# Performance work log

Hardware: AMD Instinct MI355X
Metric: run time of the kernel (lower is better)

Reference implementation:

```python
import jax, jax.numpy as jnp
import numpy as np

D_MODEL = 512
NHEAD = 4
HEAD_DIM = D_MODEL // NHEAD


def setup_inputs() -> dict:
    key = jax.random.key(0)
    ks = jax.random.split(key, 12)
    B, S = 2, 4096
    s = 1.0 / np.sqrt(D_MODEL)
    inp = {
        "query": jax.random.normal(ks[0], (B, S, D_MODEL), jnp.float32),
        "key": jax.random.normal(ks[1], (B, S, D_MODEL), jnp.float32),
        "value": jax.random.normal(ks[2], (B, S, D_MODEL), jnp.float32),
        "Wq": jax.random.uniform(ks[3], (D_MODEL, D_MODEL), jnp.float32, -s, s),
        "bq": jax.random.uniform(ks[4], (D_MODEL,), jnp.float32, -s, s),
        "Wk": jax.random.uniform(ks[5], (D_MODEL, D_MODEL), jnp.float32, -s, s),
        "bk": jax.random.uniform(ks[6], (D_MODEL,), jnp.float32, -s, s),
        "Wv": jax.random.uniform(ks[7], (D_MODEL, D_MODEL), jnp.float32, -s, s),
        "bv": jax.random.uniform(ks[8], (D_MODEL,), jnp.float32, -s, s),
        "Wo": jax.random.uniform(ks[9], (D_MODEL, D_MODEL), jnp.float32, -s, s),
        "bo": jax.random.uniform(ks[10], (D_MODEL,), jnp.float32, -s, s),
    }
    return inp


def reference(query, key, value, Wq, bq, Wk, bk, Wv, bv, Wo, bo):
    B, Sq, _ = query.shape
    Sk = key.shape[1]
    # projections (torch Linear: x @ W.T + b); split heads -> [B, H, S, hd]
    def proj(x, W, b, S):
        return (x @ W.T + b).reshape(B, S, NHEAD, HEAD_DIM).transpose(0, 2, 1, 3)
    Q = proj(query, Wq, bq, Sq)
    K = proj(key, Wk, bk, Sk)
    V = proj(value, Wv, bv, Sk)
    scale = 1.0 / np.sqrt(HEAD_DIM).astype(np.float32)
    scores = jnp.einsum("bhqd,bhkd->bhqk", Q, K) * scale  # [B,H,Sq,Sk]
    weights = jax.nn.softmax(scores, axis=-1)
    out = jnp.einsum("bhqk,bhkd->bhqd", weights, V)  # [B,H,Sq,hd]
    out = out.transpose(0, 2, 1, 3).reshape(B, Sq, D_MODEL)
    return out @ Wo.T + bo
```

## Files before the change

### kernel.cpp

```cpp
#include <hip/hip_runtime.h>


#define D_MODEL 512
#define NHEAD 4
#define HD 128
#define S_ 4096

typedef __attribute__((ext_vector_type(8))) short bf16x8;
typedef __attribute__((ext_vector_type(4))) short bf16x4;
typedef __attribute__((ext_vector_type(4))) float f32x4;
typedef __attribute__((ext_vector_type(2))) unsigned uint2v;
typedef __attribute__((ext_vector_type(4))) unsigned uint4v;

__device__ __forceinline__ short f2bf(float f) {
    unsigned u = __builtin_bit_cast(unsigned, f);
    u += 0x7fffu + ((u >> 16) & 1u);
    return (short)(u >> 16);
}
__device__ __forceinline__ unsigned pk2bf(float a, float b) {
    unsigned ua = __builtin_bit_cast(unsigned, a);
    ua += 0x7fffu + ((ua >> 16) & 1u);
    unsigned ub = __builtin_bit_cast(unsigned, b);
    ub += 0x7fffu + ((ub >> 16) & 1u);
    return (ua >> 16) | (ub & 0xffff0000u);
}
__device__ __forceinline__ void gl2lds16(const short* g, short* l) {
    __builtin_amdgcn_global_load_lds(
        (const __attribute__((address_space(1))) void*)g,
        (__attribute__((address_space(3))) void*)l, 16, 0, 0);
}

__global__ __launch_bounds__(256) void convert_kernel(
    const float* __restrict__ s0, const float* __restrict__ s1,
    const float* __restrict__ s2, const float* __restrict__ s3,
    const float* __restrict__ s4, const float* __restrict__ s5,
    const float* __restrict__ s6,
    short* __restrict__ d0, short* __restrict__ d1, short* __restrict__ d2,
    short* __restrict__ d3, short* __restrict__ d4, short* __restrict__ d5,
    short* __restrict__ d6)
{
    int seg = blockIdx.y;
    const float* src; short* dst; int n;
    const int NBIG = 2 * S_ * D_MODEL;
    const int NW = D_MODEL * D_MODEL;
    switch (seg) {
        case 0: src = s0; dst = d0; n = NBIG; break;
        case 1: src = s1; dst = d1; n = NBIG; break;
        case 2: src = s2; dst = d2; n = NBIG; break;
        case 3: src = s3; dst = d3; n = NW; break;
        case 4: src = s4; dst = d4; n = NW; break;
        case 5: src = s5; dst = d5; n = NW; break;
        default: src = s6; dst = d6; n = NW; break;
    }
    int idx = (blockIdx.x * 256 + threadIdx.x) * 8;
    if (idx >= n) return;
    float4 a = *(const float4*)(src + idx);
    float4 b = *(const float4*)(src + idx + 4);
    uint4v o;
    o[0] = pk2bf(a.x, a.y); o[1] = pk2bf(a.z, a.w);
    o[2] = pk2bf(b.x, b.y); o[3] = pk2bf(b.z, b.w);
    *(uint4v*)(dst + idx) = o;
}

__global__ __launch_bounds__(256) void qkv_kernel(
    const short* __restrict__ qb, const short* __restrict__ kb,
    const short* __restrict__ vb,
    const short* __restrict__ Wqb, const short* __restrict__ Wkb,
    const short* __restrict__ Wvb,
    const float* __restrict__ bq, const float* __restrict__ bk,
    const float* __restrict__ bv,
    short* __restrict__ Qh, short* __restrict__ Kh, short* __restrict__ VT)
{
    __shared__ short smem[12288];
    short* lA = smem;
    short* lB = smem + 4096;
    int z = blockIdx.z;
    const short* A    = (z == 0) ? qb  : (z == 1) ? kb  : vb;
    const short* W    = (z == 0) ? Wqb : (z == 1) ? Wkb : Wvb;
    const float* bias = (z == 0) ? bq  : (z == 1) ? bk  : bv;
    short* out        = (z == 0) ? Qh  : (z == 1) ? Kh  : VT;
    int vmode = (z == 2);

    int t = threadIdx.x;
    int wv = t >> 6, ln = t & 63, q4 = ln >> 4, c = ln & 15;
    int m0 = blockIdx.x * 64, n0 = blockIdx.y * 128;
    f32x4 acc[8] = {};

    for (int k0 = 0; k0 < 512; k0 += 64) {
        for (int i = 0; i < 2; ++i) {
            int id = i * 256 + t;
            int m = id >> 3, kgp = id & 7;
            gl2lds16(A + (size_t)(m0 + m) * 512 + k0 + ((kgp ^ (m & 7)) << 3),
                     &lA[id * 8]);
        }
        for (int i = 0; i < 4; ++i) {
            int id = i * 256 + t;
            int n = id >> 3, kgp = id & 7;
            gl2lds16(W + (size_t)(n0 + n) * 512 + k0 + ((kgp ^ (n & 7)) << 3),
                     &lB[id * 8]);
        }
        __syncthreads();
        for (int ks = 0; ks < 2; ++ks) {
            int kg = ks * 4 + q4;
            int m = wv * 16 + c;
            bf16x8 af = *(bf16x8*)&lA[m * 64 + ((kg ^ (m & 7)) << 3)];
            bf16x8 bfr[8];
            for (int nt = 0; nt < 8; ++nt) {
                int n = nt * 16 + c;
                bfr[nt] = *(bf16x8*)&lB[n * 64 + ((kg ^ (n & 7)) << 3)];
            }
            for (int nt = 0; nt < 8; ++nt)
                acc[nt] = __builtin_amdgcn_mfma_f32_16x16x32_bf16(af, bfr[nt], acc[nt], 0, 0, 0);
        }
        __syncthreads();
    }

    if (vmode == 0) {
        const int TS = 136;
        short* lT = smem;
        for (int nt = 0; nt < 8; ++nt) {
            float bv_ = bias[n0 + nt * 16 + c];
            for (int r = 0; r < 4; ++r) {
                int srow = wv * 16 + q4 * 4 + r;
                lT[srow * TS + nt * 16 + c] = f2bf(acc[nt][r] + bv_);
            }
        }
        __syncthreads();
        int bb = m0 >> 12, sbase = m0 & 4095, h = blockIdx.y;
        for (int i = 0; i < 4; ++i) {
            int id = i * 256 + t;
            int row = id >> 4, g = id & 15;
            bf16x8 vv = *(bf16x8*)&lT[row * TS + g * 8];
            *(bf16x8*)&out[((size_t)((bb * NHEAD + h) * S_ + sbase + row)) * HD + g * 8] = vv;
        }
    } else {
        for (int nt = 0; nt < 8; ++nt) {
            int d = nt * 16 + c;
            float bv_ = bias[n0 + d];
            uint2v pv;
            pv[0] = pk2bf(acc[nt][0] + bv_, acc[nt][1] + bv_);
            pv[1] = pk2bf(acc[nt][2] + bv_, acc[nt][3] + bv_);
            int gr = wv * 4 + q4;
            *(uint2v*)&lB[d * 64 + ((gr ^ (d & 15)) << 2)] = pv;
        }
        __syncthreads();
        int bb = m0 >> 12, sbase = m0 & 4095, h = blockIdx.y;
        for (int i = 0; i < 8; ++i) {
            int id = i * 256 + t;
            int d = id >> 4, grl = id & 15;
            bf16x4 v = *(bf16x4*)&lB[d * 64 + ((grl ^ (d & 15)) << 2)];
            *(bf16x4*)&out[((size_t)((bb * NHEAD + h) * HD + d)) * S_ + sbase + grl * 4] = v;
        }
    }
}

__global__ __launch_bounds__(256) void outproj_kernel(
    const short* __restrict__ A, const short* __restrict__ W,
    const float* __restrict__ bias, float* __restrict__ out)
{
    __shared__ short lA[64 * 64];
    __shared__ short lB[128 * 64];
    int t = threadIdx.x;
    int wv = t >> 6, ln = t & 63, q4 = ln >> 4, c = ln & 15;
    int m0 = blockIdx.x * 64, n0 = blockIdx.y * 128;
    f32x4 acc[8] = {};

    for (int k0 = 0; k0 < 512; k0 += 64) {
        for (int i = 0; i < 2; ++i) {
            int id = i * 256 + t;
            int m = id >> 3, kgp = id & 7;
            gl2lds16(A + (size_t)(m0 + m) * 512 + k0 + ((kgp ^ (m & 7)) << 3),
                     &lA[id * 8]);
        }
        for (int i = 0; i < 4; ++i) {
            int id = i * 256 + t;
            int n = id >> 3, kgp = id & 7;
            gl2lds16(W + (size_t)(n0 + n) * 512 + k0 + ((kgp ^ (n & 7)) << 3),
                     &lB[id * 8]);
        }
        __syncthreads();
        for (int ks = 0; ks < 2; ++ks) {
            int kg = ks * 4 + q4;
            int m = wv * 16 + c;
            bf16x8 af = *(bf16x8*)&lA[m * 64 + ((kg ^ (m & 7)) << 3)];
            bf16x8 bfr[8];
            for (int nt = 0; nt < 8; ++nt) {
                int n = nt * 16 + c;
                bfr[nt] = *(bf16x8*)&lB[n * 64 + ((kg ^ (n & 7)) << 3)];
            }
            for (int nt = 0; nt < 8; ++nt)
                acc[nt] = __builtin_amdgcn_mfma_f32_16x16x32_bf16(af, bfr[nt], acc[nt], 0, 0, 0);
        }
        __syncthreads();
    }

    for (int nt = 0; nt < 8; ++nt) {
        int col = n0 + nt * 16 + c;
        float bv_ = bias[col];
        for (int r = 0; r < 4; ++r) {
            int mrow = m0 + wv * 16 + q4 * 4 + r;
            out[(size_t)mrow * 512 + col] = acc[nt][r] + bv_;
        }
    }
}

__global__ __launch_bounds__(256, 2) void flash_kernel(
    const short* __restrict__ Qh, const short* __restrict__ Kh,
    const short* __restrict__ VTg, short* __restrict__ AO,
    float* __restrict__ U, float* __restrict__ ML, int nsplit, int kkspan)
{
    __shared__ short lK[64 * 128];
    __shared__ short lVT[128 * 64];
    __shared__ short lP[128 * 64];
    __shared__ float lL[2][128];
    int t = threadIdx.x;
    int wv = t >> 6, ln = t & 63, q4 = ln >> 4, c = ln & 15;
    int wi = wv >> 1, wj = wv & 1;
    int bh = blockIdx.x;
    int s0 = blockIdx.y * 128;
    int z = blockIdx.z;
    const size_t base = (size_t)bh * S_ * HD;
    const float SC = 0.08838834764831845f * 1.4426950408889634f;

    bf16x8 qf[4][4];
    for (int qt = 0; qt < 4; ++qt) {
        int s = s0 + wi * 64 + qt * 16 + c;
        const short* qp = Qh + base + (size_t)s * HD + q4 * 8;
        for (int ks = 0; ks < 4; ++ks)
            qf[qt][ks] = *(const bf16x8*)(qp + ks * 32);
    }

    f32x4 of[4][4] = {};
    float lrun[4] = {};

    int kkbeg = z * kkspan, kkend = kkbeg + kkspan;
    for (int kk0 = kkbeg; kk0 < kkend; kk0 += 64) {
        for (int i = 0; i < 4; ++i) {
            int id = i * 256 + t;
            int m = id >> 4, kgp = id & 15;
            gl2lds16(Kh + base + (size_t)(kk0 + m) * HD + ((kgp ^ (m & 7)) << 3),
                     &lK[id * 8]);
            int mv = id >> 3, kgvp = id & 7;
            gl2lds16(VTg + base + (size_t)mv * S_ + kk0 + ((kgvp ^ (mv & 7)) << 3),
                     &lVT[id * 8]);
        }
        __syncthreads();

        f32x4 sf[4][2] = {};
        for (int ks = 0; ks < 4; ++ks) {
            int kg = ks * 4 + q4;
            bf16x8 af[2];
            for (int kt = 0; kt < 2; ++kt) {
                int row = wj * 32 + kt * 16 + c;
                af[kt] = *(bf16x8*)&lK[row * 128 + ((kg ^ (row & 7)) << 3)];
            }
            for (int qt = 0; qt < 4; ++qt)
                for (int kt = 0; kt < 2; ++kt)
                    sf[qt][kt] = __builtin_amdgcn_mfma_f32_16x16x32_bf16(
                        af[kt], qf[qt][ks], sf[qt][kt], 0, 0, 0);
        }

        for (int qt = 0; qt < 4; ++qt) {
            float lt = 0.f;
            int row = wi * 64 + qt * 16 + c;
            for (int kt = 0; kt < 2; ++kt) {
                float p0 = exp2f(sf[qt][kt][0] * SC);
                float p1 = exp2f(sf[qt][kt][1] * SC);
                float p2 = exp2f(sf[qt][kt][2] * SC);
                float p3 = exp2f(sf[qt][kt][3] * SC);
                lt += (p0 + p1) + (p2 + p3);
                uint2v pv;
                pv[0] = pk2bf(p0, p1);
                pv[1] = pk2bf(p2, p3);
                int g = wj * 4 + kt * 2 + (q4 >> 1);
                *(uint2v*)&lP[row * 64 + ((g ^ (row & 7)) << 3) + ((q4 & 1) << 2)] = pv;
            }
            lt += __shfl_xor(lt, 16);
            lt += __shfl_xor(lt, 32);
            if (q4 == 0) lL[wj][wi * 64 + qt * 16 + c] = lt;
        }
        __syncthreads();

        for (int qt = 0; qt < 4; ++qt) {
            int q = wi * 64 + qt * 16 + c;
            lrun[qt] += lL[0][q] + lL[1][q];
        }

        for (int ksv = 0; ksv < 2; ++ksv) {
            int kg = ksv * 4 + q4;
            bf16x8 av[4], bp[4];
            for (int dt = 0; dt < 4; ++dt) {
                int row = wj * 64 + dt * 16 + c;
                av[dt] = *(bf16x8*)&lVT[row * 64 + ((kg ^ (row & 7)) << 3)];
            }
            for (int qt = 0; qt < 4; ++qt) {
                int row = wi * 64 + qt * 16 + c;
                bp[qt] = *(bf16x8*)&lP[row * 64 + ((kg ^ (row & 7)) << 3)];
            }
            for (int qt = 0; qt < 4; ++qt)
                for (int dt = 0; dt < 4; ++dt)
                    of[dt][qt] = __builtin_amdgcn_mfma_f32_16x16x32_bf16(
                        av[dt], bp[qt], of[dt][qt], 0, 0, 0);
        }
        __syncthreads();
    }

    if (nsplit > 1) {
        for (int qt = 0; qt < 4; ++qt) {
            int s = s0 + wi * 64 + qt * 16 + c;
            size_t rowu = (size_t)(z * 8 + bh) * S_ + s;
            float* up = U + rowu * HD;
            for (int dt = 0; dt < 4; ++dt)
                *(f32x4*)&up[wj * 64 + dt * 16 + q4 * 4] = of[dt][qt];
            if (q4 == 0 && wj == 0) ML[rowu] = lrun[qt];
        }
    } else {
        int b = bh >> 2, h = bh & 3;
        for (int qt = 0; qt < 4; ++qt) {
            float inv = 1.0f / lrun[qt];
            int s = s0 + wi * 64 + qt * 16 + c;
            short* dst = AO + ((size_t)(b * S_ + s)) * D_MODEL + h * HD;
            for (int dt = 0; dt < 4; ++dt) {
                uint2v ov;
                ov[0] = pk2bf(of[dt][qt][0] * inv, of[dt][qt][1] * inv);
                ov[1] = pk2bf(of[dt][qt][2] * inv, of[dt][qt][3] * inv);
                *(uint2v*)(dst + wj * 64 + dt * 16 + q4 * 4) = ov;
            }
        }
    }
}

__global__ __launch_bounds__(256) void combine_kernel(
    const float* __restrict__ U, const float* __restrict__ ML,
    short* __restrict__ AO)
{
    int row = blockIdx.x * 8 + (threadIdx.x >> 5);
    int d4 = (threadIdx.x & 31) * 4;
    const int R = 8 * S_;
    float l = ML[row] + ML[(size_t)R + row];
    float inv = 1.0f / l;
    f32x4 u0 = *(const f32x4*)&U[(size_t)row * HD + d4];
    f32x4 u1 = *(const f32x4*)&U[((size_t)R + row) * HD + d4];
    uint2v o;
    o[0] = pk2bf((u0[0] + u1[0]) * inv, (u0[1] + u1[1]) * inv);
    o[1] = pk2bf((u0[2] + u1[2]) * inv, (u0[3] + u1[3]) * inv);
    int bh = row >> 12, s = row & 4095;
    int b = bh >> 2, h = bh & 3;
    *(uint2v*)&AO[((size_t)(b * S_ + s)) * D_MODEL + h * HD + d4] = o;
}

extern "C" void kernel_launch(void* const* d_in, const int* in_sizes, int n_in,
                              void* d_out, int out_size, void* d_ws, size_t ws_size,
                              hipStream_t stream) {
    const float* q  = (const float*)d_in[0];
    const float* k  = (const float*)d_in[1];
    const float* v  = (const float*)d_in[2];
    const float* Wq = (const float*)d_in[3];
    const float* bq = (const float*)d_in[4];
    const float* Wk = (const float*)d_in[5];
    const float* bk = (const float*)d_in[6];
    const float* Wv = (const float*)d_in[7];
    const float* bv = (const float*)d_in[8];
    const float* Wo = (const float*)d_in[9];
    const float* bo = (const float*)d_in[10];

    const size_t HS = (size_t)2 * NHEAD * S_ * HD;
    const size_t NBIG = HS;
    const size_t NW = (size_t)D_MODEL * D_MODEL;

    char* wsb = (char*)d_ws;
    short* Qh = (short*)wsb;
    short* Kh = Qh + HS;
    short* VT = Kh + HS;
    short* AO = VT + HS;
    char* r2 = wsb + 4 * HS * 2;
    short* qb  = (short*)r2;
    short* kb  = qb + NBIG;
    short* vb  = kb + NBIG;
    short* Wqb = vb + NBIG;
    short* Wkb = Wqb + NW;
    short* Wvb = Wkb + NW;
    float* U   = (float*)r2;
    size_t r2sz = 2 * HS * 4;
    float* ML  = (float*)(r2 + r2sz);
    short* Wob = (short*)((char*)ML + (size_t)2 * 8 * S_ * 4);
    const size_t NEED = 4 * HS * 2 + r2sz + (size_t)2 * 8 * S_ * 4 + NW * 2;

    int nsplit = (ws_size >= NEED) ? 2 : 1;
    int kkspan = S_ / nsplit;

    dim3 blk(256);
    convert_kernel<<<dim3(2048, 7), blk, 0, stream>>>(
        q, k, v, Wq, Wk, Wv, Wo, qb, kb, vb, Wqb, Wkb, Wvb, Wob);
    qkv_kernel<<<dim3(128, 4, 3), blk, 0, stream>>>(
        qb, kb, vb, Wqb, Wkb, Wvb, bq, bk, bv, Qh, Kh, VT);
    flash_kernel<<<dim3(8, 32, nsplit), blk, 0, stream>>>(
        Qh, Kh, VT, AO, U, ML, nsplit, kkspan);
    if (nsplit == 2)
        combine_kernel<<<dim3(S_), blk, 0, stream>>>(U, ML, AO);
    outproj_kernel<<<dim3(128, 4), blk, 0, stream>>>(AO, Wob, bo, (float*)d_out);
}
```

Measured before the change: 260.3 us.

## Fold softmax scale into Q projection and allow four-way KV split

```diff
diff --git a/kernel.cpp b/kernel.cpp
--- a/kernel.cpp
+++ b/kernel.cpp
@@ -11,6 +11,8 @@
 typedef __attribute__((ext_vector_type(4))) float f32x4;
 typedef __attribute__((ext_vector_type(2))) unsigned uint2v;
 typedef __attribute__((ext_vector_type(4))) unsigned uint4v;
+
+#define SCQ (0.08838834764831845f * 1.4426950408889634f)
 
 __device__ __forceinline__ short f2bf(float f) {
     unsigned u = __builtin_bit_cast(unsigned, f);
@@ -80,6 +82,7 @@
     const float* bias = (z == 0) ? bq  : (z == 1) ? bk  : bv;
     short* out        = (z == 0) ? Qh  : (z == 1) ? Kh  : VT;
     int vmode = (z == 2);
+    float osc = (z == 0) ? SCQ : 1.0f;
 
     int t = threadIdx.x;
     int wv = t >> 6, ln = t & 63, q4 = ln >> 4, c = ln & 15;
@@ -122,7 +125,7 @@
             float bv_ = bias[n0 + nt * 16 + c];
             for (int r = 0; r < 4; ++r) {
                 int srow = wv * 16 + q4 * 4 + r;
-                lT[srow * TS + nt * 16 + c] = f2bf(acc[nt][r] + bv_);
+                lT[srow * TS + nt * 16 + c] = f2bf((acc[nt][r] + bv_) * osc);
             }
         }
         __syncthreads();
@@ -220,7 +223,6 @@
     int s0 = blockIdx.y * 128;
     int z = blockIdx.z;
     const size_t base = (size_t)bh * S_ * HD;
-    const float SC = 0.08838834764831845f * 1.4426950408889634f;
 
     bf16x8 qf[4][4];
     for (int qt = 0; qt < 4; ++qt) {
@@ -264,10 +266,10 @@
             float lt = 0.f;
             int row = wi * 64 + qt * 16 + c;
             for (int kt = 0; kt < 2; ++kt) {
-                float p0 = exp2f(sf[qt][kt][0] * SC);
-                float p1 = exp2f(sf[qt][kt][1] * SC);
-                float p2 = exp2f(sf[qt][kt][2] * SC);
-                float p3 = exp2f(sf[qt][kt][3] * SC);
+                float p0 = exp2f(sf[qt][kt][0]);
+                float p1 = exp2f(sf[qt][kt][1]);
+                float p2 = exp2f(sf[qt][kt][2]);
+                float p3 = exp2f(sf[qt][kt][3]);
                 lt += (p0 + p1) + (p2 + p3);
                 uint2v pv;
                 pv[0] = pk2bf(p0, p1);
@@ -332,18 +334,22 @@
 
 __global__ __launch_bounds__(256) void combine_kernel(
     const float* __restrict__ U, const float* __restrict__ ML,
-    short* __restrict__ AO)
+    short* __restrict__ AO, int nsplit)
 {
     int row = blockIdx.x * 8 + (threadIdx.x >> 5);
     int d4 = (threadIdx.x & 31) * 4;
     const int R = 8 * S_;
-    float l = ML[row] + ML[(size_t)R + row];
+    float l = 0.f;
+    f32x4 u = {0.f, 0.f, 0.f, 0.f};
+    for (int zz = 0; zz < nsplit; ++zz) {
+        l += ML[(size_t)zz * R + row];
+        f32x4 uz = *(const f32x4*)&U[((size_t)zz * R + row) * HD + d4];
+        u += uz;
+    }
     float inv = 1.0f / l;
-    f32x4 u0 = *(const f32x4*)&U[(size_t)row * HD + d4];
-    f32x4 u1 = *(const f32x4*)&U[((size_t)R + row) * HD + d4];
     uint2v o;
-    o[0] = pk2bf((u0[0] + u1[0]) * inv, (u0[1] + u1[1]) * inv);
-    o[1] = pk2bf((u0[2] + u1[2]) * inv, (u0[3] + u1[3]) * inv);
+    o[0] = pk2bf(u[0] * inv, u[1] * inv);
+    o[1] = pk2bf(u[2] * inv, u[3] * inv);
     int bh = row >> 12, s = row & 4095;
     int b = bh >> 2, h = bh & 3;
     *(uint2v*)&AO[((size_t)(b * S_ + s)) * D_MODEL + h * HD + d4] = o;
@@ -367,6 +373,7 @@
     const size_t HS = (size_t)2 * NHEAD * S_ * HD;
     const size_t NBIG = HS;
     const size_t NW = (size_t)D_MODEL * D_MODEL;
+    const size_t R = (size_t)8 * S_;
 
     char* wsb = (char*)d_ws;
     short* Qh = (short*)wsb;
@@ -381,12 +388,17 @@
     short* Wkb = Wqb + NW;
     short* Wvb = Wkb + NW;
     float* U   = (float*)r2;
-    size_t r2sz = 2 * HS * 4;
+
+    int nsplit = 1;
+    size_t r2sz = 3 * NBIG * 2 + 3 * NW * 2;
+    for (int cand = 4; cand >= 2; cand -= 2) {
+        size_t r2c = (size_t)cand * R * HD * 4;
+        if (r2c < 3 * NBIG * 2 + 3 * NW * 2) r2c = 3 * NBIG * 2 + 3 * NW * 2;
+        size_t need = 4 * HS * 2 + r2c + (size_t)cand * R * 4 + NW * 2;
+        if (ws_size >= need) { nsplit = cand; r2sz = r2c; break; }
+    }
     float* ML  = (float*)(r2 + r2sz);
-    short* Wob = (short*)((char*)ML + (size_t)2 * 8 * S_ * 4);
-    const size_t NEED = 4 * HS * 2 + r2sz + (size_t)2 * 8 * S_ * 4 + NW * 2;
-
-    int nsplit = (ws_size >= NEED) ? 2 : 1;
+    short* Wob = (short*)((char*)ML + (size_t)nsplit * R * 4);
     int kkspan = S_ / nsplit;
 
     dim3 blk(256);
@@ -396,7 +408,7 @@
         qb, kb, vb, Wqb, Wkb, Wvb, bq, bk, bv, Qh, Kh, VT);
     flash_kernel<<<dim3(8, 32, nsplit), blk, 0, stream>>>(
         Qh, Kh, VT, AO, U, ML, nsplit, kkspan);
-    if (nsplit == 2)
-        combine_kernel<<<dim3(S_), blk, 0, stream>>>(U, ML, AO);
+    if (nsplit > 1)
+        combine_kernel<<<dim3(S_), blk, 0, stream>>>(U, ML, AO, nsplit);
     outproj_kernel<<<dim3(128, 4), blk, 0, stream>>>(AO, Wob, bo, (float*)d_out);
 }
```

Result: faster. 252.6 us (-2.9%).
